# Kernel optimization log

Hardware: AMD Instinct MI355X
Metric: run time of the kernel (lower is better)

The kernel has to match this reference:

```python
import jax, jax.numpy as jnp
import numpy as np

B, T, F = 2048, 336, 10
H1, H2, D1, D2 = 70, 21, 30, 20


def _lstm_dir(xg, w_hh):
    """Run one LSTM direction. xg: [T, B, 4H] = x@W_ih^T + b_ih + b_hh (precomputed).
    Gate order matches PyTorch: i, f, g, o."""
    H = w_hh.shape[1]
    h0 = jnp.zeros((xg.shape[1], H), xg.dtype)

    def step(carry, g_in):
        h, c = carry
        g = g_in + h @ w_hh.T
        i, f, gg, o = jnp.split(g, 4, axis=-1)
        c = jax.nn.sigmoid(f) * c + jax.nn.sigmoid(i) * jnp.tanh(gg)
        h = jax.nn.sigmoid(o) * jnp.tanh(c)
        return (h, c), h

    _, hs = jax.lax.scan(step, (h0, h0), xg)
    return hs  # [T, B, H]


def _bilstm(x, wf_ih, wf_hh, bf_ih, bf_hh, wb_ih, wb_hh, bb_ih, bb_hh):
    """Bidirectional LSTM, batch_first in/out. x: [B, T, I] -> [B, T, 2H]."""
    xt = x.transpose(1, 0, 2)  # [T, B, I]
    gf = xt @ wf_ih.T + (bf_ih + bf_hh)
    hf = _lstm_dir(gf, wf_hh)
    gb = (xt @ wb_ih.T + (bb_ih + bb_hh))[::-1]
    hb = _lstm_dir(gb, wb_hh)[::-1]
    return jnp.concatenate([hf, hb], axis=-1).transpose(1, 0, 2)


def setup_inputs() -> dict:
    key = jax.random.key(0)
    ks = iter(jax.random.split(key, 32))

    def u(shape, h):  # PyTorch default init: U(-1/sqrt(H), 1/sqrt(H))
        s = 1.0 / np.sqrt(h)
        return jax.random.uniform(next(ks), shape, jnp.float32, -s, s)

    inp = {"x": jax.random.normal(next(ks), (B, T, F), jnp.float32)}
    # lstm1: input F, hidden H1, bidirectional
    for d in ("f", "b"):
        inp[f"w1{d}_ih"] = u((4 * H1, F), H1)
        inp[f"w1{d}_hh"] = u((4 * H1, H1), H1)
        inp[f"b1{d}_ih"] = u((4 * H1,), H1)
        inp[f"b1{d}_hh"] = u((4 * H1,), H1)
    # lstm2: input 2*H1, hidden H2, bidirectional
    for d in ("f", "b"):
        inp[f"w2{d}_ih"] = u((4 * H2, 2 * H1), H2)
        inp[f"w2{d}_hh"] = u((4 * H2, H2), H2)
        inp[f"b2{d}_ih"] = u((4 * H2,), H2)
        inp[f"b2{d}_hh"] = u((4 * H2,), H2)
    # dense head
    inp["wd1"] = u((D1, 2 * H2), 2 * H2)
    inp["bd1"] = u((D1,), 2 * H2)
    inp["wd2"] = u((D2, D1), D1)
    inp["bd2"] = u((D2,), D1)
    inp["wo"] = u((1, D2), D2)
    inp["bo"] = u((1,), D2)
    return inp


def reference(x,
              w1f_ih, w1f_hh, b1f_ih, b1f_hh, w1b_ih, w1b_hh, b1b_ih, b1b_hh,
              w2f_ih, w2f_hh, b2f_ih, b2f_hh, w2b_ih, w2b_hh, b2b_ih, b2b_hh,
              wd1, bd1, wd2, bd2, wo, bo):
    h = _bilstm(x, w1f_ih, w1f_hh, b1f_ih, b1f_hh, w1b_ih, w1b_hh, b1b_ih, b1b_hh)
    h = _bilstm(h, w2f_ih, w2f_hh, b2f_ih, b2f_hh, w2b_ih, w2b_hh, b2b_ih, b2b_hh)
    h = jax.nn.relu(h @ wd1.T + bd1)
    h = jax.nn.relu(h @ wd2.T + bd2)
    return h @ wo.T + bo  # [B, T, 1]
```

## Files before the change

kernel.cpp:

```cpp
#include <hip/hip_runtime.h>

#define Bz 2048
#define Tz 336
#define Fz 10
#define H1 70
#define H2 21

typedef __attribute__((ext_vector_type(8))) short short8;
typedef __attribute__((ext_vector_type(4))) float float4v;

#define MFMA16(a, b, c) __builtin_amdgcn_mfma_f32_16x16x32_bf16((a), (b), (c), 0, 0, 0)

__device__ __forceinline__ void sync_lds() {
    asm volatile("s_waitcnt lgkmcnt(0)\n\ts_barrier" ::: "memory");
}

__device__ __forceinline__ unsigned short f2bf(float v) {
    unsigned int u = __float_as_uint(v);
    u += 0x7FFFu + ((u >> 16) & 1u);
    return (unsigned short)(u >> 16);
}
__device__ __forceinline__ float bf2f(unsigned short s) {
    return __uint_as_float(((unsigned int)s) << 16);
}

__device__ __forceinline__ float lstm_gate_h(float gi, float gf, float gc,
                                             float go, float& cst) {
    float a  = __expf(-gf);
    float b  = __expf(-gi);
    float d  = __expf(2.0f * gc);
    float pa = 1.0f + a;
    float pb = 1.0f + b;
    float pd = d + 1.0f;
    float t1 = pb * pd;
    float num = fmaf(pa, d - 1.0f, cst * t1);
    float cn  = num / (pa * t1);
    float e2  = __expf(-go);
    float f2  = __expf(2.0f * cn);
    float h   = (f2 - 1.0f) / ((1.0f + e2) * (f2 + 1.0f));
    cst = cn;
    return h;
}

__device__ __forceinline__ int frag_off(int m, int k) {
    return (k >> 3) * 128 + m * 8 + (k & 7);
}

__global__ __launch_bounds__(1024, 4) void k_lstm1(
    const float* __restrict__ x,
    const float* __restrict__ wih_f, const float* __restrict__ whh_f,
    const float* __restrict__ bih_f, const float* __restrict__ bhh_f,
    const float* __restrict__ wih_b, const float* __restrict__ whh_b,
    const float* __restrict__ bih_b, const float* __restrict__ bhh_b,
    unsigned short* __restrict__ y1)
{
    __shared__ short hB_hi[2][1536];

    const int tb  = blockIdx.x & 127;
    const int dir = blockIdx.x >> 7;
    const int b0  = tb << 4;
    const float* wih = dir ? wih_b : wih_f;
    const float* whh = dir ? whh_b : whh_f;
    const float* bih = dir ? bih_b : bih_f;
    const float* bhh = dir ? bhh_b : bhh_f;

    const int tid  = threadIdx.x;
    const int wv   = tid >> 6;
    const int lane = tid & 63;
    const int n    = lane & 15;
    const int quad = lane >> 4;
    const int NT1  = (wv < 2) ? 2 : 1;

    short8 whi[2][3], wlo[2][3];
    const int g_ = n & 3;
#pragma unroll
    for (int tt = 0; tt < 2; ++tt) {
        if (tt < NT1) {
            const int p  = wv + 16 * tt;
            const int uu = 4 * p + (n >> 2);
#pragma unroll
            for (int q = 0; q < 3; ++q) {
#pragma unroll
                for (int j = 0; j < 8; ++j) {
                    int k = q * 32 + quad * 8 + j;
                    float v = 0.0f;
                    if (uu < H1) {
                        int row = g_ * H1 + uu;
                        if (k < H1)        v = whh[row * H1 + k];
                        else if (k < 80)   v = wih[row * Fz + (k - H1)];
                        else if (k == 80)  v = bih[row] + bhh[row];
                    }
                    unsigned short hi = f2bf(v);
                    unsigned short lo = f2bf(v - bf2f(hi));
                    whi[tt][q][j] = (short)hi;
                    wlo[tt][q][j] = (short)lo;
                }
            }
        }
    }

    for (int e = tid; e < 1536; e += 1024) {
        hB_hi[0][e] = 0; hB_hi[1][e] = 0;
    }
    __syncthreads();
    if (tid < 16) {
        int off = 1280 + tid * 8;
        hB_hi[0][off] = (short)0x3F80;
        hB_hi[1][off] = (short)0x3F80;
    }

    const int es = tid - 864;
    const bool stg = (es >= 0 && es < 160);
    int sm = 0, sf = 0;
    if (stg) { sm = es / Fz; sf = es % Fz; }

    const int tstep = dir ? -1 : 1;
    const int t0    = dir ? (Tz - 1) : 0;

    float xv = 0.0f;
    if (stg) {
        float v = x[((size_t)(b0 + sm) * Tz + t0) * Fz + sf];
        hB_hi[0][frag_off(sm, H1 + sf)] = (short)f2bf(v);
        xv = x[((size_t)(b0 + sm) * Tz + t0 + tstep) * Fz + sf];
    }
    const float* xp = x + ((size_t)(b0 + sm) * Tz + t0 + 2 * tstep) * Fz + sf;
    const ptrdiff_t xinc = (ptrdiff_t)tstep * Fz;
    unsigned short* yp = y1 + (((size_t)t0 * 128 + tb) * 140 + dir * H1) * 16 + n;
    const ptrdiff_t yinc = (ptrdiff_t)tstep * (140 * 128 * 16);

    const int xoff = frag_off(sm, H1 + sf);
    int hoff[2];
#pragma unroll
    for (int tt = 0; tt < 2; ++tt) hoff[tt] = frag_off(n, 4 * (wv + 16 * tt) + quad);

    float cst[2];
    cst[0] = 0.0f; cst[1] = 0.0f;

    auto body = [&](int step, const int pp) __attribute__((always_inline)) {
        sync_lds();

        if (stg && step + 1 < Tz) {
            hB_hi[pp ^ 1][xoff] = (short)f2bf(xv);
        }
        if (stg && step + 2 < Tz) {
            xv = *xp;
        }

        short8 bhi[3];
#pragma unroll
        for (int q = 0; q < 3; ++q)
            bhi[q] = *(const short8*)&hB_hi[pp][q * 512 + lane * 8];

        float4v acc[2];
#pragma unroll
        for (int tt = 0; tt < 2; ++tt) acc[tt] = (float4v){0.f, 0.f, 0.f, 0.f};
#pragma unroll
        for (int tt = 0; tt < 2; ++tt) {
            if (tt < NT1) {
                acc[tt] = MFMA16(whi[tt][0], bhi[0], acc[tt]);
                acc[tt] = MFMA16(wlo[tt][0], bhi[0], acc[tt]);
                acc[tt] = MFMA16(whi[tt][1], bhi[1], acc[tt]);
                acc[tt] = MFMA16(wlo[tt][1], bhi[1], acc[tt]);
                acc[tt] = MFMA16(whi[tt][2], bhi[2], acc[tt]);
                acc[tt] = MFMA16(wlo[tt][2], bhi[2], acc[tt]);
            }
        }

#pragma unroll
        for (int tt = 0; tt < 2; ++tt) {
            if (tt < NT1) {
                const int u = 4 * (wv + 16 * tt) + quad;
                if (u < H1) {
                    float h = lstm_gate_h(acc[tt][0], acc[tt][1],
                                          acc[tt][2], acc[tt][3], cst[tt]);
                    unsigned short hh = f2bf(h);
                    hB_hi[pp ^ 1][hoff[tt]] = (short)hh;
                    yp[u * 16] = hh;
                }
            }
        }
        xp += xinc;
        yp += yinc;
    };

    for (int step = 0; step < Tz; step += 2) {
        body(step, 0);
        body(step + 1, 1);
    }
}

__global__ __launch_bounds__(512, 2) void k_lstm2(
    const unsigned short* __restrict__ y1,
    const float* __restrict__ wih_f, const float* __restrict__ whh_f,
    const float* __restrict__ bih_f, const float* __restrict__ bhh_f,
    const float* __restrict__ wih_b, const float* __restrict__ whh_b,
    const float* __restrict__ bih_b, const float* __restrict__ bhh_b,
    unsigned short* __restrict__ y2)
{
    __shared__ short hB_hi[2][3072];

    const int tb  = blockIdx.x & 127;
    const int dir = blockIdx.x >> 7;
    const int b0  = tb << 4;
    const float* wih = dir ? wih_b : wih_f;
    const float* whh = dir ? whh_b : whh_f;
    const float* bih = dir ? bih_b : bih_f;
    const float* bhh = dir ? bhh_b : bhh_f;

    const int tid  = threadIdx.x;
    const int wv   = tid >> 6;
    const int lane = tid & 63;
    const int n    = lane & 15;
    const int quad = lane >> 4;
    const bool comp = (wv < 6);

    short8 whi[6], wlo0;
    const int g_ = n & 3;
    if (comp) {
        const int uu = 4 * wv + (n >> 2);
#pragma unroll
        for (int q = 0; q < 6; ++q) {
#pragma unroll
            for (int j = 0; j < 8; ++j) {
                int k = q * 32 + quad * 8 + j;
                float v = 0.0f;
                if (uu < H2) {
                    int row = g_ * H2 + uu;
                    if (k < H2)                   v = whh[row * H2 + k];
                    else if (k == 21)             v = bih[row] + bhh[row];
                    else if (k >= 32 && k < 172)  v = wih[row * 140 + (k - 32)];
                }
                unsigned short hi = f2bf(v);
                whi[q][j] = (short)hi;
                if (q == 0) wlo0[j] = (short)f2bf(v - bf2f(hi));
            }
        }
    }

    for (int e = tid; e < 3072; e += 512) { hB_hi[0][e] = 0; hB_hi[1][e] = 0; }
    __syncthreads();
    if (tid < 16) {
        int off = frag_off(tid, 21);
        hB_hi[0][off] = (short)0x3F80;
        hB_hi[1][off] = (short)0x3F80;
    }

    const int es = tid - 232;
    const bool stg = (es >= 0 && es < 280);

    const int tstep = dir ? -1 : 1;
    const int t0    = dir ? (Tz - 1) : 0;

    short8 xr = (short8){0,0,0,0,0,0,0,0};
    if (stg) {
        short8 v = *(const short8*)(y1 + ((size_t)t0 * 128 + tb) * 2240 + es * 8);
#pragma unroll
        for (int j = 0; j < 8; ++j) {
            int idx = es * 8 + j;
            hB_hi[0][frag_off(idx & 15, 32 + (idx >> 4))] = v[j];
        }
        xr = *(const short8*)(y1 + ((size_t)(t0 + tstep) * 128 + tb) * 2240 + es * 8);
    }
    const unsigned short* srcp =
        y1 + ((size_t)(t0 + 2 * tstep) * 128 + tb) * 2240 + es * 8;
    const ptrdiff_t sinc = (ptrdiff_t)tstep * (128 * 2240);
    unsigned short* yp2 = y2 + ((size_t)(b0 + n) * Tz + t0) * 42 + dir * H2;
    const ptrdiff_t yinc = (ptrdiff_t)tstep * 42;

    int xoffs[8];
#pragma unroll
    for (int j = 0; j < 8; ++j) {
        int idx = es * 8 + j;
        xoffs[j] = frag_off(idx & 15, 32 + (idx >> 4));
    }
    const int u     = 4 * wv + quad;
    const int hoffc = frag_off(n, (u < H2) ? u : 0);

    float cst = 0.0f;

    auto body = [&](int step, const int pp) __attribute__((always_inline)) {
        sync_lds();

        if (stg && step + 1 < Tz) {
#pragma unroll
            for (int j = 0; j < 8; ++j)
                hB_hi[pp ^ 1][xoffs[j]] = xr[j];
        }
        if (stg && step + 2 < Tz) {
            xr = *(const short8*)srcp;
        }

        if (comp) {
            short8 bhi[6];
#pragma unroll
            for (int q = 0; q < 6; ++q)
                bhi[q] = *(const short8*)&hB_hi[pp][q * 512 + lane * 8];

            float4v acc = (float4v){0.f, 0.f, 0.f, 0.f};
            acc = MFMA16(whi[0], bhi[0], acc);
            acc = MFMA16(wlo0,   bhi[0], acc);
            acc = MFMA16(whi[1], bhi[1], acc);
            acc = MFMA16(whi[2], bhi[2], acc);
            acc = MFMA16(whi[3], bhi[3], acc);
            acc = MFMA16(whi[4], bhi[4], acc);
            acc = MFMA16(whi[5], bhi[5], acc);

            if (u < H2) {
                float h = lstm_gate_h(acc[0], acc[1], acc[2], acc[3], cst);
                unsigned short hh = f2bf(h);
                hB_hi[pp ^ 1][hoffc] = (short)hh;
                yp2[u] = hh;
            }
        }
        srcp += sinc;
        yp2  += yinc;
    };

    for (int step = 0; step < Tz; step += 2) {
        body(step, 0);
        body(step + 1, 1);
    }
}

__global__ __launch_bounds__(256) void k_dense(
    const unsigned short* __restrict__ y2,
    const float* __restrict__ wd1, const float* __restrict__ bd1,
    const float* __restrict__ wd2, const float* __restrict__ bd2,
    const float* __restrict__ wo,  const float* __restrict__ bo,
    float* __restrict__ out)
{
    int idx = blockIdx.x * 256 + threadIdx.x;
    if (idx >= Bz * Tz) return;
    const unsigned int* row = (const unsigned int*)&y2[(size_t)idx * 42];

    float v[42];
#pragma unroll
    for (int j = 0; j < 21; ++j) {
        unsigned int p = row[j];
        v[2 * j]     = bf2f((unsigned short)(p & 0xFFFFu));
        v[2 * j + 1] = bf2f((unsigned short)(p >> 16));
    }

    float h1[30];
#pragma unroll
    for (int o = 0; o < 30; ++o) {
        float s = bd1[o];
#pragma unroll
        for (int j = 0; j < 42; ++j) s = fmaf(v[j], wd1[o * 42 + j], s);
        h1[o] = fmaxf(s, 0.0f);
    }
    float outv = bo[0];
#pragma unroll
    for (int o = 0; o < 20; ++o) {
        float s = bd2[o];
#pragma unroll
        for (int j = 0; j < 30; ++j) s = fmaf(h1[j], wd2[o * 30 + j], s);
        outv = fmaf(fmaxf(s, 0.0f), wo[o], outv);
    }
    out[idx] = outv;
}

extern "C" void kernel_launch(void* const* d_in, const int* in_sizes, int n_in,
                              void* d_out, int out_size, void* d_ws, size_t ws_size,
                              hipStream_t stream)
{
    const float* x      = (const float*)d_in[0];
    const float* w1f_ih = (const float*)d_in[1];
    const float* w1f_hh = (const float*)d_in[2];
    const float* b1f_ih = (const float*)d_in[3];
    const float* b1f_hh = (const float*)d_in[4];
    const float* w1b_ih = (const float*)d_in[5];
    const float* w1b_hh = (const float*)d_in[6];
    const float* b1b_ih = (const float*)d_in[7];
    const float* b1b_hh = (const float*)d_in[8];
    const float* w2f_ih = (const float*)d_in[9];
    const float* w2f_hh = (const float*)d_in[10];
    const float* b2f_ih = (const float*)d_in[11];
    const float* b2f_hh = (const float*)d_in[12];
    const float* w2b_ih = (const float*)d_in[13];
    const float* w2b_hh = (const float*)d_in[14];
    const float* b2b_ih = (const float*)d_in[15];
    const float* b2b_hh = (const float*)d_in[16];
    const float* wd1    = (const float*)d_in[17];
    const float* bd1    = (const float*)d_in[18];
    const float* wd2    = (const float*)d_in[19];
    const float* bd2    = (const float*)d_in[20];
    const float* wo     = (const float*)d_in[21];
    const float* bo     = (const float*)d_in[22];
    float* out = (float*)d_out;

    const size_t y1_elems = (size_t)Tz * 128 * 2240;
    const size_t y2_elems = (size_t)Bz * Tz * 42;
    if (ws_size < (y1_elems + y2_elems) * 2) return;

    unsigned short* y1 = (unsigned short*)d_ws;
    unsigned short* y2 = y1 + y1_elems;

    hipLaunchKernelGGL(k_lstm1, dim3(256), dim3(1024), 0, stream,
                       x, w1f_ih, w1f_hh, b1f_ih, b1f_hh,
                       w1b_ih, w1b_hh, b1b_ih, b1b_hh, y1);
    hipLaunchKernelGGL(k_lstm2, dim3(256), dim3(512), 0, stream,
                       y1, w2f_ih, w2f_hh, b2f_ih, b2f_hh,
                       w2b_ih, w2b_hh, b2b_ih, b2b_hh, y2);
    hipLaunchKernelGGL(k_dense, dim3((Bz * Tz + 255) / 256), dim3(256), 0, stream,
                       y2, wd1, bd1, wd2, bd2, wo, bo, out);
}
```

Before: 582.1 us.

## Store layer-1 output in MFMA fragment layout so layer-2 stages with vector LDS writes

Layer 1 now writes its hidden outputs directly into the LDS fragment layout that layer 2's MFMA B-operand expects, padded to 2304 elements per time/batch tile. Layer 2 can then copy each 8-element global chunk into LDS with one 16-byte store instead of eight scattered 2-byte stores, zeroing a small hole region. This cuts LDS store instructions and index math in layer 2's per-step critical path, at the cost of a slightly larger workspace and a more scattered global write pattern in layer 1.

```diff
diff --git a/kernel.cpp b/kernel.cpp
--- a/kernel.cpp
+++ b/kernel.cpp
@@ -125,13 +125,18 @@
     }
     const float* xp = x + ((size_t)(b0 + sm) * Tz + t0 + 2 * tstep) * Fz + sf;
     const ptrdiff_t xinc = (ptrdiff_t)tstep * Fz;
-    unsigned short* yp = y1 + (((size_t)t0 * 128 + tb) * 140 + dir * H1) * 16 + n;
-    const ptrdiff_t yinc = (ptrdiff_t)tstep * (140 * 128 * 16);
+    unsigned short* ypB = y1 + (size_t)(t0 * 128 + tb) * 2304;
+    const ptrdiff_t yinc = (ptrdiff_t)tstep * (128 * 2304);
 
     const int xoff = frag_off(sm, H1 + sf);
-    int hoff[2];
-#pragma unroll
-    for (int tt = 0; tt < 2; ++tt) hoff[tt] = frag_off(n, 4 * (wv + 16 * tt) + quad);
+    int hoff[2], yoff[2];
+#pragma unroll
+    for (int tt = 0; tt < 2; ++tt) {
+        const int u = 4 * (wv + 16 * tt) + quad;
+        hoff[tt] = frag_off(n, u);
+        const int K = 32 + dir * H1 + u;
+        yoff[tt] = ((K >> 3) * 16 + n) * 8 + (K & 7) - 512;
+    }
 
     float cst[2];
     cst[0] = 0.0f; cst[1] = 0.0f;
@@ -175,12 +180,12 @@
                                           acc[tt][2], acc[tt][3], cst[tt]);
                     unsigned short hh = f2bf(h);
                     hB_hi[pp ^ 1][hoff[tt]] = (short)hh;
-                    yp[u * 16] = hh;
+                    ypB[yoff[tt]] = hh;
                 }
             }
         }
-        xp += xinc;
-        yp += yinc;
+        xp  += xinc;
+        ypB += yinc;
     };
 
     for (int step = 0; step < Tz; step += 2) {
@@ -245,34 +250,26 @@
         hB_hi[1][off] = (short)0x3F80;
     }
 
-    const int es = tid - 232;
-    const bool stg = (es >= 0 && es < 280);
+    const int es = tid - 224;
+    const bool stg = (es >= 0 && es < 288);
+    const bool hole = (es >= 272);
 
     const int tstep = dir ? -1 : 1;
     const int t0    = dir ? (Tz - 1) : 0;
 
     short8 xr = (short8){0,0,0,0,0,0,0,0};
     if (stg) {
-        short8 v = *(const short8*)(y1 + ((size_t)t0 * 128 + tb) * 2240 + es * 8);
-#pragma unroll
-        for (int j = 0; j < 8; ++j) {
-            int idx = es * 8 + j;
-            hB_hi[0][frag_off(idx & 15, 32 + (idx >> 4))] = v[j];
-        }
-        xr = *(const short8*)(y1 + ((size_t)(t0 + tstep) * 128 + tb) * 2240 + es * 8);
+        short8 v = *(const short8*)(y1 + ((size_t)t0 * 128 + tb) * 2304 + es * 8);
+        if (hole) { v[4] = 0; v[5] = 0; v[6] = 0; v[7] = 0; }
+        *(short8*)&hB_hi[0][512 + es * 8] = v;
+        xr = *(const short8*)(y1 + ((size_t)(t0 + tstep) * 128 + tb) * 2304 + es * 8);
     }
     const unsigned short* srcp =
-        y1 + ((size_t)(t0 + 2 * tstep) * 128 + tb) * 2240 + es * 8;
-    const ptrdiff_t sinc = (ptrdiff_t)tstep * (128 * 2240);
+        y1 + ((size_t)(t0 + 2 * tstep) * 128 + tb) * 2304 + es * 8;
+    const ptrdiff_t sinc = (ptrdiff_t)tstep * (128 * 2304);
     unsigned short* yp2 = y2 + ((size_t)(b0 + n) * Tz + t0) * 42 + dir * H2;
     const ptrdiff_t yinc = (ptrdiff_t)tstep * 42;
 
-    int xoffs[8];
-#pragma unroll
-    for (int j = 0; j < 8; ++j) {
-        int idx = es * 8 + j;
-        xoffs[j] = frag_off(idx & 15, 32 + (idx >> 4));
-    }
     const int u     = 4 * wv + quad;
     const int hoffc = frag_off(n, (u < H2) ? u : 0);
 
@@ -282,9 +279,9 @@
         sync_lds();
 
         if (stg && step + 1 < Tz) {
-#pragma unroll
-            for (int j = 0; j < 8; ++j)
-                hB_hi[pp ^ 1][xoffs[j]] = xr[j];
+            short8 v = xr;
+            if (hole) { v[4] = 0; v[5] = 0; v[6] = 0; v[7] = 0; }
+            *(short8*)&hB_hi[pp ^ 1][512 + es * 8] = v;
         }
         if (stg && step + 2 < Tz) {
             xr = *(const short8*)srcp;
@@ -389,7 +386,7 @@
     const float* bo     = (const float*)d_in[22];
     float* out = (float*)d_out;
 
-    const size_t y1_elems = (size_t)Tz * 128 * 2240;
+    const size_t y1_elems = (size_t)Tz * 128 * 2304;
     const size_t y2_elems = (size_t)Bz * Tz * 42;
     if (ws_size < (y1_elems + y2_elems) * 2) return;
 
```

Measured after the change: 574.4 us (median of 2 runs). About the same (-1.3%).
